# Performance work log

Measured on AMD Instinct MI355X. Metric: run time of the kernel, lower is better.

## Reference

```python
import jax, jax.numpy as jnp
import numpy as np

SEQ_LEN = 4096
D_MODEL = 768
N_Q = 8
Q_DIM = D_MODEL // N_Q  # 96
WINDOW = 128


def apply_rope(x, theta):
    # x: [L, d]; standard rotary embedding on even/odd pairs.
    L = x.shape[0]
    pos = jnp.arange(L, dtype=x.dtype)
    ang = pos[:, None] * theta[None, :]              # [L, d/2]
    cos, sin = jnp.cos(ang), jnp.sin(ang)
    x_even, x_odd = x[:, 0::2], x[:, 1::2]
    out_even = x_even * cos - x_odd * sin
    out_odd = x_even * sin + x_odd * cos
    return jnp.stack([out_even, out_odd], axis=-1).reshape(x.shape)


def setup_inputs() -> dict:
    key = jax.random.key(0)
    kx, kw1, kb1, kw2, kb2 = jax.random.split(key, 5)
    s_in = 1.0 / np.sqrt(D_MODEL)
    return {
        "x": jax.random.normal(kx, (SEQ_LEN, D_MODEL), dtype=jnp.float32),
        "Wqkv": jax.random.normal(kw1, (Q_DIM * (N_Q + 2), D_MODEL), dtype=jnp.float32) * s_in,
        "bqkv": jax.random.normal(kb1, (Q_DIM * (N_Q + 2),), dtype=jnp.float32) * s_in,
        "Wout": jax.random.normal(kw2, (D_MODEL, D_MODEL), dtype=jnp.float32) * s_in,
        "bout": jax.random.normal(kb2, (D_MODEL,), dtype=jnp.float32) * s_in,
    }


def reference(x, Wqkv, bqkv, Wout, bout):
    L = x.shape[0]
    qkv = x @ Wqkv.T + bqkv                                   # [L, 10*Q_DIM]
    k = qkv[:, :Q_DIM]                                        # [L, Q_DIM]
    v = qkv[:, Q_DIM:2 * Q_DIM]                               # [L, Q_DIM]
    q = qkv[:, 2 * Q_DIM:].reshape(L, N_Q, Q_DIM)             # [L, H, Q_DIM]

    theta = 1.0 / 10000.0 ** (jnp.arange(0, Q_DIM, 2, dtype=jnp.float32) / Q_DIM)
    q = jax.vmap(lambda h: apply_rope(h, theta), in_axes=1, out_axes=1)(q)
    k = apply_rope(k, theta)

    # Banded causal mask: j <= i and j > i - WINDOW
    i = jnp.arange(L)[:, None]
    j = jnp.arange(L)[None, :]
    mask = (j <= i) & (j > i - WINDOW)                        # [L, L] bool

    # NOTE: source multiplies by sqrt(q_dim) (faithful to original code).
    scores = jnp.sqrt(jnp.float32(Q_DIM)) * jnp.einsum('ihd,jd->hij', q, k)  # [H, L, L]
    scores = jnp.where(mask[None, :, :], scores, -jnp.inf)
    attn = jax.nn.softmax(scores, axis=2)                     # each row has >=1 valid (diag)

    out = jnp.einsum('hij,jd->hid', attn, v)                  # [H, L, Q_DIM]
    out = out.transpose(1, 0, 2).reshape(L, -1)               # [L, D_MODEL]
    return out @ Wout.T + bout
```

## Files before the change

### kernel.cpp

```cpp
#include <hip/hip_runtime.h>

typedef _Float16 f16;
typedef _Float16 half8 __attribute__((ext_vector_type(8)));
typedef _Float16 f16x2 __attribute__((ext_vector_type(2)));
typedef _Float16 f16x4 __attribute__((ext_vector_type(4)));
typedef float    f32x4 __attribute__((ext_vector_type(4)));

#define DM    768
#define QD    96
#define MFMA16(a,b,c) __builtin_amdgcn_mfma_f32_16x16x32_f16(a, b, c, 0, 0, 0)

__device__ __forceinline__ void async_copy16(const f16* g, f16* l) {
  __builtin_amdgcn_global_load_lds((const __attribute__((address_space(1))) void*)g,
                                   (__attribute__((address_space(3))) void*)l,
                                   16, 0, 0);
}

__global__ __launch_bounds__(256) void prep_kernel(const float* __restrict__ x,
                                                   const float* __restrict__ Wqkv,
                                                   const float* __restrict__ bqkv,
                                                   const float* __restrict__ Wout,
                                                   f16* __restrict__ xh,
                                                   f16* __restrict__ w1h,
                                                   f16* __restrict__ w2h,
                                                   float* __restrict__ b1p,
                                                   float* __restrict__ ctab,
                                                   float* __restrict__ stab) {
  const int NW1 = 1024 * 768 / 4;
  const int NW2 = 768 * 768 / 4;
  int b = blockIdx.x;
  if (b < 3072) {
    int idx = b * 256 + threadIdx.x;
    f32x4 v = ((const f32x4*)x)[idx];
    f16x4 o;
    o[0] = (f16)v[0]; o[1] = (f16)v[1]; o[2] = (f16)v[2]; o[3] = (f16)v[3];
    ((f16x4*)xh)[idx] = o;
    return;
  }
  if (b < 4420) {
    int idx = (b - 3072) * 256 + threadIdx.x;
    if (idx < NW1) {
      int r = idx / 192;
      f16x4 o;
      if (r < 960) {
        f32x4 v = ((const f32x4*)Wqkv)[idx];
        o[0] = (f16)v[0]; o[1] = (f16)v[1]; o[2] = (f16)v[2]; o[3] = (f16)v[3];
      } else {
        o[0] = (f16)0.f; o[1] = (f16)0.f; o[2] = (f16)0.f; o[3] = (f16)0.f;
      }
      ((f16x4*)w1h)[idx] = o;
    } else if (idx < NW1 + NW2) {
      int j = idx - NW1;
      f32x4 v = ((const f32x4*)Wout)[j];
      f16x4 o;
      o[0] = (f16)v[0]; o[1] = (f16)v[1]; o[2] = (f16)v[2]; o[3] = (f16)v[3];
      ((f16x4*)w2h)[j] = o;
    } else {
      int j = idx - (NW1 + NW2);
      b1p[j] = (j < 960) ? bqkv[j] : 0.f;
    }
    return;
  }
  int idx = (b - 4420) * 256 + threadIdx.x;
  int pos = idx >> 6, f = idx & 63;
  if (f < 48) {
    float theta = exp2f((float)f * -0.27682734f);
    float s, c;
    sincosf((float)pos * theta, &s, &c);
    ctab[pos * 48 + f] = c;
    stab[pos * 48 + f] = s;
  }
}

#define GEMM_VM5  asm volatile("s_waitcnt vmcnt(5)" ::: "memory")
#define GEMM_VM0  asm volatile("s_waitcnt vmcnt(0)" ::: "memory")
#define GEMM_SB   __builtin_amdgcn_s_barrier()
#define GEMM_SCB  __builtin_amdgcn_sched_barrier(0)

#define GEMM_STAGE(BUF, K0)                                         \
  do {                                                              \
    async_copy16(Ap + (K0),           lA0 + (BUF) * 2048);          \
    async_copy16(Bp + (K0),           lB0 + (BUF) * 8192);          \
    async_copy16(Bp + 32 * K + (K0),  lB0 + (BUF) * 8192 + 2048);   \
    async_copy16(Bp + 64 * K + (K0),  lB0 + (BUF) * 8192 + 4096);   \
    async_copy16(Bp + 96 * K + (K0),  lB0 + (BUF) * 8192 + 6144);   \
  } while (0)

#define GEMM_COMPUTE(BUF)                                                      \
  do {                                                                         \
    half8 a[2][2], b[2][2];                                                    \
    _Pragma("unroll")                                                          \
    for (int m = 0; m < 2; ++m) {                                              \
      int row = m * 16 + fr;                                                   \
      _Pragma("unroll")                                                        \
      for (int kk = 0; kk < 2; ++kk) {                                         \
        int c = (kk << 2) | kg;                                                \
        a[m][kk] = *(const half8*)&As[BUF][row * 64 + ((c ^ (row & 7)) << 3)]; \
      }                                                                        \
    }                                                                          \
    _Pragma("unroll")                                                          \
    for (int n = 0; n < 2; ++n) {                                              \
      int row = w * 32 + n * 16 + fr;                                          \
      _Pragma("unroll")                                                        \
      for (int kk = 0; kk < 2; ++kk) {                                         \
        int c = (kk << 2) | kg;                                                \
        b[n][kk] = *(const half8*)&Bs[BUF][row * 64 + ((c ^ (row & 7)) << 3)]; \
      }                                                                        \
    }                                                                          \
    _Pragma("unroll")                                                          \
    for (int m = 0; m < 2; ++m)                                                \
      _Pragma("unroll")                                                        \
      for (int n = 0; n < 2; ++n) {                                            \
        acc[m][n] = MFMA16(a[m][0], b[n][0], acc[m][n]);                       \
        acc[m][n] = MFMA16(a[m][1], b[n][1], acc[m][n]);                       \
      }                                                                        \
  } while (0)

#define GEMM_PROLOGUE_AND_LOOP                                      \
  __shared__ f16 As[2][32 * 64];                                    \
  __shared__ f16 Bs[2][128 * 64];                                   \
  const int t  = threadIdx.x;                                       \
  const int bm = blockIdx.x * 32;                                   \
  const int bn = blockIdx.y * 128;                                  \
  const int w  = t >> 6, l = t & 63;                                \
  const int fr = l & 15, kg = l >> 4;                               \
  f32x4 acc[2][2] = {};                                             \
  const int srow = t >> 3;                                          \
  const int skc  = ((t & 7) ^ (srow & 7)) << 3;   \
  const f16* Ap = A + (size_t)(bm + srow) * K + skc;                \
  const f16* Bp = B + (size_t)(bn + srow) * K + skc;                \
  f16* lA0 = &As[0][t * 8];                                         \
  f16* lB0 = &Bs[0][t * 8];                                         \
  const int nt = K >> 6;                                  \
  GEMM_STAGE(0, 0);                                                 \
  GEMM_STAGE(1, 64);                                                \
  for (int tk = 0; tk < nt; ++tk) {                                 \
    if (tk + 1 < nt) { GEMM_VM5; } else { GEMM_VM0; }               \
    GEMM_SB; GEMM_SCB;                                              \
    GEMM_COMPUTE(tk & 1);                                           \
    GEMM_SCB; GEMM_SB;                                              \
    if (tk + 2 < nt) GEMM_STAGE(tk & 1, (tk + 2) << 6);             \
  }

__global__ __launch_bounds__(256) void gemm_f16_tn(const f16* __restrict__ A,
                                                   const f16* __restrict__ B,
                                                   const float* __restrict__ bias,
                                                   float* __restrict__ C,
                                                   int K, int ldc) {
  GEMM_PROLOGUE_AND_LOOP
  const int r0 = kg * 4;
#pragma unroll
  for (int n = 0; n < 2; ++n) {
    int col = bn + w * 32 + n * 16 + fr;
    float bv = bias[col];
#pragma unroll
    for (int m = 0; m < 2; ++m) {
      int row = bm + m * 16 + r0;
#pragma unroll
      for (int r = 0; r < 4; ++r)
        C[(size_t)(row + r) * ldc + col] = acc[m][n][r] + bv;
    }
  }
}

__global__ __launch_bounds__(256) void gemm_qkv_rope(const f16* __restrict__ A,
                                                     const f16* __restrict__ B,
                                                     const float* __restrict__ bias,
                                                     const float* __restrict__ ctab,
                                                     const float* __restrict__ stab,
                                                     f16* __restrict__ qh,
                                                     f16* __restrict__ ql,
                                                     f16* __restrict__ kh,
                                                     f16* __restrict__ kl,
                                                     f16* __restrict__ vT) {
  const int K = 768;
  GEMM_PROLOGUE_AND_LOOP
  const int r0 = kg * 4;
  f16* ls = &As[0][0];
  const int vlo = (bn < 96) ? 96 : bn;
  const int vhi = (bn + 128 < 192) ? (bn + 128) : 192;
  const bool has_v = vlo < vhi;
  const bool even = !(fr & 1);
#pragma unroll
  for (int n = 0; n < 2; ++n) {
    int col = bn + w * 32 + n * 16 + fr;
    float bv = bias[col];
    int seg = (col * 683) >> 16;
    int f = (col - seg * 96) >> 1;
#pragma unroll
    for (int m = 0; m < 2; ++m) {
      int row = bm + m * 16 + r0;
      if (seg == 1) {
        f16x4 pk;
#pragma unroll
        for (int r = 0; r < 4; ++r) pk[r] = (f16)(acc[m][n][r] + bv);
        *(f16x4*)&ls[(col - vlo) * 40 + m * 16 + r0] = pk;
        continue;
      }
#pragma unroll
      for (int r = 0; r < 4; ++r) {
        float v = acc[m][n][r] + bv;
        float p = __shfl_xor(v, 1);
        if (even && col < 960) {
          float c = ctab[(row + r) * 48 + f];
          float s = stab[(row + r) * 48 + f];
          float re = v * c - p * s;
          float ro = v * s + p * c;
          f16 hie = (f16)re, hio = (f16)ro;
          f16x2 hv; hv[0] = hie; hv[1] = hio;
          f16x2 lv; lv[0] = (f16)(re - (float)hie); lv[1] = (f16)(ro - (float)hio);
          if (seg == 0) {
            *(f16x2*)(kh + (size_t)(row + r) * QD + col) = hv;
            *(f16x2*)(kl + (size_t)(row + r) * QD + col) = lv;
          } else {
            int qc = col - 192;
            *(f16x2*)(qh + (size_t)(row + r) * DM + qc) = hv;
            *(f16x2*)(ql + (size_t)(row + r) * DM + qc) = lv;
          }
        }
      }
    }
  }
  if (has_v) {
    __syncthreads();
    const int nv = vhi - vlo;
    for (int idx = t; idx < nv * 4; idx += 256) {
      int cl = idx >> 2, sg = idx & 3;
      *(half8*)(vT + (size_t)(vlo - 96 + cl) * 4096 + bm + sg * 8) =
          *(half8*)&ls[cl * 40 + sg * 8];
    }
  }
}

__global__ __launch_bounds__(256) void attn2_kernel(const f16* __restrict__ qh,
                                                    const f16* __restrict__ ql,
                                                    const f16* __restrict__ kh,
                                                    const f16* __restrict__ kl,
                                                    const f16* __restrict__ vT,
                                                    f16* __restrict__ aout) {
  __shared__ f16 kbuf[192 * 104];
  __shared__ f16 klbuf[192 * 104];
  __shared__ f16 vbuf[96 * 200];
  __shared__ f16 pbuf[4][32 * 40];
  const int t  = threadIdx.x, w = t >> 6, l = t & 63;
  const int fr = l & 15, kg = l >> 4;
  const int i0 = blockIdx.x * 64;
  const int h  = blockIdx.y * 2 + (w >> 1);
  const int q0 = (w & 1) * 32;
  const int jbase = i0 - 128;
  const int nlo = (w & 1) ? 2 : 0;

  for (int it = 0; it < 9; ++it) {
    int c = t + 256 * it;
    int row = c / 12, seg = c - row * 12;
    int jabs = jbase + row; if (jabs < 0) jabs = 0;
    *(half8*)(kbuf + row * 104 + seg * 8) =
        *(const half8*)(kh + (size_t)jabs * QD + seg * 8);
    *(half8*)(klbuf + row * 104 + seg * 8) =
        *(const half8*)(kl + (size_t)jabs * QD + seg * 8);
  }
  for (int it = 0; it < 9; ++it) {
    int c = t + 256 * it;
    int row = c / 24, seg = c - row * 24;
    int col0 = jbase + seg * 8; if (col0 < 0) col0 = 0;
    *(half8*)(vbuf + row * 200 + seg * 8) =
        *(const half8*)(vT + (size_t)row * 4096 + col0);
  }

  half8 a_h[2][3], a_l[2][3];
#pragma unroll
  for (int m = 0; m < 2; ++m) {
    size_t qoff = (size_t)(i0 + q0 + m * 16 + fr) * DM + h * QD;
#pragma unroll
    for (int kc = 0; kc < 3; ++kc) {
      a_h[m][kc] = *(const half8*)(qh + qoff + kc * 32 + kg * 8);
      a_l[m][kc] = *(const half8*)(ql + qoff + kc * 32 + kg * 8);
    }
  }
  __syncthreads();

  f32x4 s[2][12];
#pragma unroll
  for (int m = 0; m < 2; ++m)
#pragma unroll
    for (int n = 0; n < 12; ++n)
      s[m][n] = (f32x4){0.f, 0.f, 0.f, 0.f};

  __builtin_amdgcn_s_setprio(1);
#pragma unroll
  for (int n = 0; n < 12; ++n) {
    if (n < nlo || n >= nlo + 10) continue;
    int krow = n * 16 + fr;
#pragma unroll
    for (int kc = 0; kc < 3; ++kc) {
      half8 b_h = *(const half8*)(kbuf + krow * 104 + kc * 32 + kg * 8);
      half8 b_l = *(const half8*)(klbuf + krow * 104 + kc * 32 + kg * 8);
      s[0][n] = MFMA16(a_h[0][kc], b_h, s[0][n]);
      s[1][n] = MFMA16(a_h[1][kc], b_h, s[1][n]);
      s[0][n] = MFMA16(a_l[0][kc], b_h, s[0][n]);
      s[1][n] = MFMA16(a_l[1][kc], b_h, s[1][n]);
      s[0][n] = MFMA16(a_h[0][kc], b_l, s[0][n]);
      s[1][n] = MFMA16(a_h[1][kc], b_l, s[1][n]);
    }
  }
  __builtin_amdgcn_s_setprio(0);

  const int jmin = (i0 < 128) ? (128 - i0) : 0;
  const float scale = 9.79795897113271f;
  float mx[2][4], sm[2][4], inv[2][4];
#pragma unroll
  for (int m = 0; m < 2; ++m)
#pragma unroll
    for (int r = 0; r < 4; ++r) mx[m][r] = -1e30f;

#pragma unroll
  for (int m = 0; m < 2; ++m)
#pragma unroll
    for (int n = 0; n < 12; ++n) {
      if (n < nlo || n >= nlo + 10) continue;
      int jloc = n * 16 + fr;
#pragma unroll
      for (int r = 0; r < 4; ++r) {
        int iloc = q0 + m * 16 + kg * 4 + r;
        bool valid = (jloc > iloc) && (jloc <= iloc + 128) && (jloc >= jmin);
        float v = valid ? s[m][n][r] * scale : -1e30f;
        s[m][n][r] = v;
        mx[m][r] = fmaxf(mx[m][r], v);
      }
    }
#pragma unroll
  for (int m = 0; m < 2; ++m)
#pragma unroll
    for (int r = 0; r < 4; ++r) {
      float v = mx[m][r];
      v = fmaxf(v, __shfl_xor(v, 1));
      v = fmaxf(v, __shfl_xor(v, 2));
      v = fmaxf(v, __shfl_xor(v, 4));
      v = fmaxf(v, __shfl_xor(v, 8));
      mx[m][r] = v;
      sm[m][r] = 0.f;
    }
#pragma unroll
  for (int m = 0; m < 2; ++m)
#pragma unroll
    for (int n = 0; n < 12; ++n) {
      if (n < nlo || n >= nlo + 10) continue;
#pragma unroll
      for (int r = 0; r < 4; ++r) {
        float p = __expf(s[m][n][r] - mx[m][r]);
        s[m][n][r] = p;
        sm[m][r] += p;
      }
    }
#pragma unroll
  for (int m = 0; m < 2; ++m)
#pragma unroll
    for (int r = 0; r < 4; ++r) {
      float v = sm[m][r];
      v += __shfl_xor(v, 1);
      v += __shfl_xor(v, 2);
      v += __shfl_xor(v, 4);
      v += __shfl_xor(v, 8);
      inv[m][r] = 1.f / v;
    }

  f16* pw = pbuf[w];
  const int c6lo = nlo >> 1;
  f32x4 o[2][6];
#pragma unroll
  for (int m = 0; m < 2; ++m)
#pragma unroll
    for (int dn = 0; dn < 6; ++dn)
      o[m][dn] = (f32x4){0.f, 0.f, 0.f, 0.f};

#pragma unroll
  for (int c6 = 0; c6 < 6; ++c6) {
    if (c6 < c6lo || c6 >= c6lo + 5) continue;
#pragma unroll
    for (int m = 0; m < 2; ++m)
#pragma unroll
      for (int nn = 0; nn < 2; ++nn)
#pragma unroll
        for (int r = 0; r < 4; ++r)
          pw[(m * 16 + kg * 4 + r) * 40 + nn * 16 + fr] = (f16)s[m][2 * c6 + nn][r];
    half8 ap0 = *(half8*)(pw + fr * 40 + kg * 8);
    half8 ap1 = *(half8*)(pw + (16 + fr) * 40 + kg * 8);
    __builtin_amdgcn_s_setprio(1);
#pragma unroll
    for (int dn = 0; dn < 6; ++dn) {
      half8 bv = *(half8*)(vbuf + (dn * 16 + fr) * 200 + c6 * 32 + kg * 8);
      o[0][dn] = MFMA16(ap0, bv, o[0][dn]);
      o[1][dn] = MFMA16(ap1, bv, o[1][dn]);
    }
    __builtin_amdgcn_s_setprio(0);
  }

#pragma unroll
  for (int m = 0; m < 2; ++m)
#pragma unroll
    for (int dn = 0; dn < 6; ++dn) {
      int col = h * QD + dn * 16 + fr;
#pragma unroll
      for (int r = 0; r < 4; ++r) {
        int row = i0 + q0 + m * 16 + kg * 4 + r;
        aout[(size_t)row * DM + col] = (f16)(o[m][dn][r] * inv[m][r]);
      }
    }
}

extern "C" void kernel_launch(void* const* d_in, const int* in_sizes, int n_in,
                              void* d_out, int out_size, void* d_ws, size_t ws_size,
                              hipStream_t stream) {
  const float* x    = (const float*)d_in[0];
  const float* Wqkv = (const float*)d_in[1];
  const float* bqkv = (const float*)d_in[2];
  const float* Wout = (const float*)d_in[3];
  const float* bout = (const float*)d_in[4];
  float* out = (float*)d_out;

  char* ws = (char*)d_ws;
  f16*   xh   = (f16*)(ws);
  f16*   w1h  = (f16*)(ws + 6291456);
  f16*   w2h  = (f16*)(ws + 7864320);
  float* b1p  = (float*)(ws + 9043968);
  float* ctab = (float*)(ws + 9048064);
  float* stab = (float*)(ws + 9834496);
  f16*   qh   = (f16*)(ws + 10620928);
  f16*   ql   = (f16*)(ws + 16912384);
  f16*   kh   = (f16*)(ws + 23203840);
  f16*   kl   = (f16*)(ws + 23990272);
  f16*   vT   = (f16*)(ws + 24776704);
  f16*   aout = (f16*)(ws + 25563136);

  prep_kernel<<<dim3(5444), dim3(256), 0, stream>>>(x, Wqkv, bqkv, Wout,
                                                    xh, w1h, w2h, b1p, ctab, stab);
  gemm_qkv_rope<<<dim3(128, 8), dim3(256), 0, stream>>>(xh, w1h, b1p, ctab, stab,
                                                        qh, ql, kh, kl, vT);
  attn2_kernel<<<dim3(64, 4), dim3(256), 0, stream>>>(qh, ql, kh, kl, vT, aout);
  gemm_f16_tn<<<dim3(128, 6), dim3(256), 0, stream>>>(aout, w2h, bout, out, 768, 768);
}
```

Measured before the change: 54.92 us.

## Load GEMM A operand directly into double-buffered registers, bypassing LDS

The A tile of the shared GEMM mainloop is no longer staged through LDS with async copies. Each lane now reads its MFMA A fragments straight from global memory into two register buffers that alternate between iterations, and the vmcnt wait is retuned to match the new load counts. This removes the LDS writes and reads for A and frees that LDS space; the QKV epilogue now reuses the B buffer as scratch instead. In exchange, all four waves fetch the same A rows, so global/L2 traffic for A rises, the per-lane row-strided loads coalesce less well, and register pressure goes up.

Result: slower. 83.86 us (+52.7%).

```diff
diff --git a/kernel.cpp b/kernel.cpp
--- a/kernel.cpp
+++ b/kernel.cpp
@@ -72,32 +72,32 @@
   }
 }
 
-#define GEMM_VM5  asm volatile("s_waitcnt vmcnt(5)" ::: "memory")
+#define GEMM_VM4  asm volatile("s_waitcnt vmcnt(4)" ::: "memory")
 #define GEMM_VM0  asm volatile("s_waitcnt vmcnt(0)" ::: "memory")
 #define GEMM_SB   __builtin_amdgcn_s_barrier()
 #define GEMM_SCB  __builtin_amdgcn_sched_barrier(0)
 
-#define GEMM_STAGE(BUF, K0)                                         \
+#define GEMM_STAGE_B(BUF, K0)                                       \
   do {                                                              \
-    async_copy16(Ap + (K0),           lA0 + (BUF) * 2048);          \
     async_copy16(Bp + (K0),           lB0 + (BUF) * 8192);          \
     async_copy16(Bp + 32 * K + (K0),  lB0 + (BUF) * 8192 + 2048);   \
     async_copy16(Bp + 64 * K + (K0),  lB0 + (BUF) * 8192 + 4096);   \
     async_copy16(Bp + 96 * K + (K0),  lB0 + (BUF) * 8192 + 6144);   \
   } while (0)
 
-#define GEMM_COMPUTE(BUF)                                                      \
+#define GEMM_LOAD_A(REG, K0)                                        \
+  do {                                                              \
+    _Pragma("unroll")                                               \
+    for (int m = 0; m < 2; ++m)                                     \
+      _Pragma("unroll")                                             \
+      for (int kk = 0; kk < 2; ++kk)                                \
+        REG[m][kk] = *(const half8*)(Aq + (size_t)(m * 16) * K +    \
+                                     (K0) + (((kk << 2) | kg) << 3)); \
+  } while (0)
+
+#define GEMM_COMPUTE(BUF, AREG)                                                \
   do {                                                                         \
-    half8 a[2][2], b[2][2];                                                    \
-    _Pragma("unroll")                                                          \
-    for (int m = 0; m < 2; ++m) {                                              \
-      int row = m * 16 + fr;                                                   \
-      _Pragma("unroll")                                                        \
-      for (int kk = 0; kk < 2; ++kk) {                                         \
-        int c = (kk << 2) | kg;                                                \
-        a[m][kk] = *(const half8*)&As[BUF][row * 64 + ((c ^ (row & 7)) << 3)]; \
-      }                                                                        \
-    }                                                                          \
+    half8 b[2][2];                                                             \
     _Pragma("unroll")                                                          \
     for (int n = 0; n < 2; ++n) {                                              \
       int row = w * 32 + n * 16 + fr;                                          \
@@ -111,13 +111,12 @@
     for (int m = 0; m < 2; ++m)                                                \
       _Pragma("unroll")                                                        \
       for (int n = 0; n < 2; ++n) {                                            \
-        acc[m][n] = MFMA16(a[m][0], b[n][0], acc[m][n]);                       \
-        acc[m][n] = MFMA16(a[m][1], b[n][1], acc[m][n]);                       \
+        acc[m][n] = MFMA16(AREG[m][0], b[n][0], acc[m][n]);                    \
+        acc[m][n] = MFMA16(AREG[m][1], b[n][1], acc[m][n]);                    \
       }                                                                        \
   } while (0)
 
 #define GEMM_PROLOGUE_AND_LOOP                                      \
-  __shared__ f16 As[2][32 * 64];                                    \
   __shared__ f16 Bs[2][128 * 64];                                   \
   const int t  = threadIdx.x;                                       \
   const int bm = blockIdx.x * 32;                                   \
@@ -127,19 +126,24 @@
   f32x4 acc[2][2] = {};                                             \
   const int srow = t >> 3;                                          \
   const int skc  = ((t & 7) ^ (srow & 7)) << 3;   \
-  const f16* Ap = A + (size_t)(bm + srow) * K + skc;                \
   const f16* Bp = B + (size_t)(bn + srow) * K + skc;                \
-  f16* lA0 = &As[0][t * 8];                                         \
+  const f16* Aq = A + (size_t)(bm + fr) * K;                        \
   f16* lB0 = &Bs[0][t * 8];                                         \
-  const int nt = K >> 6;                                  \
-  GEMM_STAGE(0, 0);                                                 \
-  GEMM_STAGE(1, 64);                                                \
+  const int nt = K >> 6;                            \
+  half8 a0[2][2], a1[2][2];                                         \
+  GEMM_STAGE_B(0, 0);                                               \
+  GEMM_LOAD_A(a0, 0);                                               \
+  GEMM_STAGE_B(1, 64);                                              \
   for (int tk = 0; tk < nt; ++tk) {                                 \
-    if (tk + 1 < nt) { GEMM_VM5; } else { GEMM_VM0; }               \
+    if (tk + 1 < nt) { GEMM_VM4; } else { GEMM_VM0; }               \
     GEMM_SB; GEMM_SCB;                                              \
-    GEMM_COMPUTE(tk & 1);                                           \
+    if (tk & 1) { GEMM_COMPUTE(1, a1); } else { GEMM_COMPUTE(0, a0); } \
     GEMM_SCB; GEMM_SB;                                              \
-    if (tk + 2 < nt) GEMM_STAGE(tk & 1, (tk + 2) << 6);             \
+    if (tk + 1 < nt) {                                              \
+      if (tk & 1) { GEMM_LOAD_A(a0, (tk + 1) << 6); }               \
+      else        { GEMM_LOAD_A(a1, (tk + 1) << 6); }               \
+    }                                                               \
+    if (tk + 2 < nt) GEMM_STAGE_B(tk & 1, (tk + 2) << 6);           \
   }
 
 __global__ __launch_bounds__(256) void gemm_f16_tn(const f16* __restrict__ A,
@@ -176,7 +180,7 @@
   const int K = 768;
   GEMM_PROLOGUE_AND_LOOP
   const int r0 = kg * 4;
-  f16* ls = &As[0][0];
+  f16* ls = &Bs[0][0];
   const int vlo = (bn < 96) ? 96 : bn;
   const int vhi = (bn + 128 < 192) ? (bn + 128) : 192;
   const bool has_v = vlo < vhi;
```

## Halve attention query tile per block and shrink LDS footprint

Applied to the files above, without the earlier changes.

The attention kernel now handles 32 query rows per block instead of 64, which doubles the grid to 128x4 blocks and halves the per-wave accumulator registers. The low K part is no longer staged in LDS and is read straight from global memory. The P staging buffer reuses the K buffer after a barrier, which cuts LDS use and should raise occupancy. In exchange, K and V window data is loaded redundantly across more blocks, and the k-low reads from global add latency to the QK MFMA loop.

After: 57.28 us. +4.3%, slower.

```diff
diff --git a/kernel.cpp b/kernel.cpp
--- a/kernel.cpp
+++ b/kernel.cpp
@@ -232,180 +232,159 @@
   }
 }
 
-__global__ __launch_bounds__(256) void attn2_kernel(const f16* __restrict__ qh,
+__global__ __launch_bounds__(256) void attn3_kernel(const f16* __restrict__ qh,
                                                     const f16* __restrict__ ql,
                                                     const f16* __restrict__ kh,
                                                     const f16* __restrict__ kl,
                                                     const f16* __restrict__ vT,
                                                     f16* __restrict__ aout) {
-  __shared__ f16 kbuf[192 * 104];
-  __shared__ f16 klbuf[192 * 104];
-  __shared__ f16 vbuf[96 * 200];
-  __shared__ f16 pbuf[4][32 * 40];
+  __shared__ f16 kbuf[160 * 104];
+  __shared__ f16 vbuf[96 * 168];
   const int t  = threadIdx.x, w = t >> 6, l = t & 63;
   const int fr = l & 15, kg = l >> 4;
-  const int i0 = blockIdx.x * 64;
+  const int i0 = blockIdx.x * 32;
   const int h  = blockIdx.y * 2 + (w >> 1);
-  const int q0 = (w & 1) * 32;
+  const int q0 = (w & 1) * 16;
   const int jbase = i0 - 128;
-  const int nlo = (w & 1) ? 2 : 0;
-
-  for (int it = 0; it < 9; ++it) {
+  const int nlo = w & 1;
+
+  for (int it = 0; it < 8; ++it) {
     int c = t + 256 * it;
-    int row = c / 12, seg = c - row * 12;
-    int jabs = jbase + row; if (jabs < 0) jabs = 0;
-    *(half8*)(kbuf + row * 104 + seg * 8) =
-        *(const half8*)(kh + (size_t)jabs * QD + seg * 8);
-    *(half8*)(klbuf + row * 104 + seg * 8) =
-        *(const half8*)(kl + (size_t)jabs * QD + seg * 8);
-  }
-  for (int it = 0; it < 9; ++it) {
+    if (c < 1920) {
+      int row = c / 12, seg = c - row * 12;
+      int jabs = jbase + row; if (jabs < 0) jabs = 0;
+      *(half8*)(kbuf + row * 104 + seg * 8) =
+          *(const half8*)(kh + (size_t)jabs * QD + seg * 8);
+    }
+  }
+  for (int it = 0; it < 8; ++it) {
     int c = t + 256 * it;
-    int row = c / 24, seg = c - row * 24;
-    int col0 = jbase + seg * 8; if (col0 < 0) col0 = 0;
-    *(half8*)(vbuf + row * 200 + seg * 8) =
-        *(const half8*)(vT + (size_t)row * 4096 + col0);
-  }
-
-  half8 a_h[2][3], a_l[2][3];
-#pragma unroll
-  for (int m = 0; m < 2; ++m) {
-    size_t qoff = (size_t)(i0 + q0 + m * 16 + fr) * DM + h * QD;
+    if (c < 1920) {
+      int row = c / 20, seg = c - row * 20;
+      int col0 = jbase + seg * 8; if (col0 < 0) col0 = 0;
+      *(half8*)(vbuf + row * 168 + seg * 8) =
+          *(const half8*)(vT + (size_t)row * 4096 + col0);
+    }
+  }
+
+  half8 a_h[3], a_l[3];
+  {
+    size_t qoff = (size_t)(i0 + q0 + fr) * DM + h * QD;
 #pragma unroll
     for (int kc = 0; kc < 3; ++kc) {
-      a_h[m][kc] = *(const half8*)(qh + qoff + kc * 32 + kg * 8);
-      a_l[m][kc] = *(const half8*)(ql + qoff + kc * 32 + kg * 8);
+      a_h[kc] = *(const half8*)(qh + qoff + kc * 32 + kg * 8);
+      a_l[kc] = *(const half8*)(ql + qoff + kc * 32 + kg * 8);
     }
   }
   __syncthreads();
 
-  f32x4 s[2][12];
-#pragma unroll
-  for (int m = 0; m < 2; ++m)
-#pragma unroll
-    for (int n = 0; n < 12; ++n)
-      s[m][n] = (f32x4){0.f, 0.f, 0.f, 0.f};
+  f32x4 s[10];
+#pragma unroll
+  for (int n = 0; n < 10; ++n) s[n] = (f32x4){0.f, 0.f, 0.f, 0.f};
 
   __builtin_amdgcn_s_setprio(1);
 #pragma unroll
-  for (int n = 0; n < 12; ++n) {
-    if (n < nlo || n >= nlo + 10) continue;
+  for (int n = 0; n < 10; ++n) {
+    if (n < nlo || n >= nlo + 9) continue;
     int krow = n * 16 + fr;
+    int jabs = jbase + krow; if (jabs < 0) jabs = 0;
 #pragma unroll
     for (int kc = 0; kc < 3; ++kc) {
       half8 b_h = *(const half8*)(kbuf + krow * 104 + kc * 32 + kg * 8);
-      half8 b_l = *(const half8*)(klbuf + krow * 104 + kc * 32 + kg * 8);
-      s[0][n] = MFMA16(a_h[0][kc], b_h, s[0][n]);
-      s[1][n] = MFMA16(a_h[1][kc], b_h, s[1][n]);
-      s[0][n] = MFMA16(a_l[0][kc], b_h, s[0][n]);
-      s[1][n] = MFMA16(a_l[1][kc], b_h, s[1][n]);
-      s[0][n] = MFMA16(a_h[0][kc], b_l, s[0][n]);
-      s[1][n] = MFMA16(a_h[1][kc], b_l, s[1][n]);
+      half8 b_l = *(const half8*)(kl + (size_t)jabs * QD + kc * 32 + kg * 8);
+      s[n] = MFMA16(a_h[kc], b_h, s[n]);
+      s[n] = MFMA16(a_l[kc], b_h, s[n]);
+      s[n] = MFMA16(a_h[kc], b_l, s[n]);
     }
   }
   __builtin_amdgcn_s_setprio(0);
 
   const int jmin = (i0 < 128) ? (128 - i0) : 0;
   const float scale = 9.79795897113271f;
-  float mx[2][4], sm[2][4], inv[2][4];
-#pragma unroll
-  for (int m = 0; m < 2; ++m)
-#pragma unroll
-    for (int r = 0; r < 4; ++r) mx[m][r] = -1e30f;
-
-#pragma unroll
-  for (int m = 0; m < 2; ++m)
-#pragma unroll
-    for (int n = 0; n < 12; ++n) {
-      if (n < nlo || n >= nlo + 10) continue;
-      int jloc = n * 16 + fr;
-#pragma unroll
-      for (int r = 0; r < 4; ++r) {
-        int iloc = q0 + m * 16 + kg * 4 + r;
-        bool valid = (jloc > iloc) && (jloc <= iloc + 128) && (jloc >= jmin);
-        float v = valid ? s[m][n][r] * scale : -1e30f;
-        s[m][n][r] = v;
-        mx[m][r] = fmaxf(mx[m][r], v);
-      }
-    }
-#pragma unroll
-  for (int m = 0; m < 2; ++m)
+  float mx[4], sm[4], inv[4];
+#pragma unroll
+  for (int r = 0; r < 4; ++r) mx[r] = -1e30f;
+
+#pragma unroll
+  for (int n = 0; n < 10; ++n) {
+    if (n < nlo || n >= nlo + 9) continue;
+    int jloc = n * 16 + fr;
 #pragma unroll
     for (int r = 0; r < 4; ++r) {
-      float v = mx[m][r];
-      v = fmaxf(v, __shfl_xor(v, 1));
-      v = fmaxf(v, __shfl_xor(v, 2));
-      v = fmaxf(v, __shfl_xor(v, 4));
-      v = fmaxf(v, __shfl_xor(v, 8));
-      mx[m][r] = v;
-      sm[m][r] = 0.f;
-    }
-#pragma unroll
-  for (int m = 0; m < 2; ++m)
-#pragma unroll
-    for (int n = 0; n < 12; ++n) {
-      if (n < nlo || n >= nlo + 10) continue;
-#pragma unroll
-      for (int r = 0; r < 4; ++r) {
-        float p = __expf(s[m][n][r] - mx[m][r]);
-        s[m][n][r] = p;
-        sm[m][r] += p;
-      }
-    }
-#pragma unroll
-  for (int m = 0; m < 2; ++m)
+      int iloc = q0 + kg * 4 + r;
+      bool valid = (jloc > iloc) && (jloc <= iloc + 128) && (jloc >= jmin);
+      float v = valid ? s[n][r] * scale : -1e30f;
+      s[n][r] = v;
+      mx[r] = fmaxf(mx[r], v);
+    }
+  }
+#pragma unroll
+  for (int r = 0; r < 4; ++r) {
+    float v = mx[r];
+    v = fmaxf(v, __shfl_xor(v, 1));
+    v = fmaxf(v, __shfl_xor(v, 2));
+    v = fmaxf(v, __shfl_xor(v, 4));
+    v = fmaxf(v, __shfl_xor(v, 8));
+    mx[r] = v;
+    sm[r] = 0.f;
+  }
+#pragma unroll
+  for (int n = 0; n < 10; ++n) {
+    if (n < nlo || n >= nlo + 9) {
+#pragma unroll
+      for (int r = 0; r < 4; ++r) s[n][r] = 0.f;
+      continue;
+    }
 #pragma unroll
     for (int r = 0; r < 4; ++r) {
-      float v = sm[m][r];
-      v += __shfl_xor(v, 1);
-      v += __shfl_xor(v, 2);
-      v += __shfl_xor(v, 4);
-      v += __shfl_xor(v, 8);
-      inv[m][r] = 1.f / v;
-    }
-
-  f16* pw = pbuf[w];
-  const int c6lo = nlo >> 1;
-  f32x4 o[2][6];
-#pragma unroll
-  for (int m = 0; m < 2; ++m)
-#pragma unroll
-    for (int dn = 0; dn < 6; ++dn)
-      o[m][dn] = (f32x4){0.f, 0.f, 0.f, 0.f};
-
-#pragma unroll
-  for (int c6 = 0; c6 < 6; ++c6) {
-    if (c6 < c6lo || c6 >= c6lo + 5) continue;
-#pragma unroll
-    for (int m = 0; m < 2; ++m)
-#pragma unroll
-      for (int nn = 0; nn < 2; ++nn)
-#pragma unroll
-        for (int r = 0; r < 4; ++r)
-          pw[(m * 16 + kg * 4 + r) * 40 + nn * 16 + fr] = (f16)s[m][2 * c6 + nn][r];
-    half8 ap0 = *(half8*)(pw + fr * 40 + kg * 8);
-    half8 ap1 = *(half8*)(pw + (16 + fr) * 40 + kg * 8);
+      float p = __expf(s[n][r] - mx[r]);
+      s[n][r] = p;
+      sm[r] += p;
+    }
+  }
+#pragma unroll
+  for (int r = 0; r < 4; ++r) {
+    float v = sm[r];
+    v += __shfl_xor(v, 1);
+    v += __shfl_xor(v, 2);
+    v += __shfl_xor(v, 4);
+    v += __shfl_xor(v, 8);
+    inv[r] = 1.f / v;
+  }
+
+  __syncthreads();
+
+  f16* pw = kbuf + w * 640;
+  f32x4 o[6];
+#pragma unroll
+  for (int dn = 0; dn < 6; ++dn) o[dn] = (f32x4){0.f, 0.f, 0.f, 0.f};
+
+#pragma unroll
+  for (int c6 = 0; c6 < 5; ++c6) {
+#pragma unroll
+    for (int nn = 0; nn < 2; ++nn)
+#pragma unroll
+      for (int r = 0; r < 4; ++r)
+        pw[(kg * 4 + r) * 40 + nn * 16 + fr] = (f16)s[2 * c6 + nn][r];
+    half8 ap = *(half8*)(pw + fr * 40 + kg * 8);
     __builtin_amdgcn_s_setprio(1);
 #pragma unroll
     for (int dn = 0; dn < 6; ++dn) {
-      half8 bv = *(half8*)(vbuf + (dn * 16 + fr) * 200 + c6 * 32 + kg * 8);
-      o[0][dn] = MFMA16(ap0, bv, o[0][dn]);
-      o[1][dn] = MFMA16(ap1, bv, o[1][dn]);
+      half8 bv = *(half8*)(vbuf + (dn * 16 + fr) * 168 + c6 * 32 + kg * 8);
+      o[dn] = MFMA16(ap, bv, o[dn]);
     }
     __builtin_amdgcn_s_setprio(0);
   }
 
 #pragma unroll
-  for (int m = 0; m < 2; ++m)
-#pragma unroll
-    for (int dn = 0; dn < 6; ++dn) {
-      int col = h * QD + dn * 16 + fr;
-#pragma unroll
-      for (int r = 0; r < 4; ++r) {
-        int row = i0 + q0 + m * 16 + kg * 4 + r;
-        aout[(size_t)row * DM + col] = (f16)(o[m][dn][r] * inv[m][r]);
-      }
-    }
+  for (int dn = 0; dn < 6; ++dn) {
+    int col = h * QD + dn * 16 + fr;
+#pragma unroll
+    for (int r = 0; r < 4; ++r) {
+      int row = i0 + q0 + kg * 4 + r;
+      aout[(size_t)row * DM + col] = (f16)(o[dn][r] * inv[r]);
+    }
+  }
 }
 
 extern "C" void kernel_launch(void* const* d_in, const int* in_sizes, int n_in,
@@ -436,6 +415,6 @@
                                                     xh, w1h, w2h, b1p, ctab, stab);
   gemm_qkv_rope<<<dim3(128, 8), dim3(256), 0, stream>>>(xh, w1h, b1p, ctab, stab,
                                                         qh, ql, kh, kl, vT);
-  attn2_kernel<<<dim3(64, 4), dim3(256), 0, stream>>>(qh, ql, kh, kl, vT, aout);
+  attn3_kernel<<<dim3(128, 4), dim3(256), 0, stream>>>(qh, ql, kh, kl, vT, aout);
   gemm_f16_tn<<<dim3(128, 6), dim3(256), 0, stream>>>(aout, w2h, bout, out, 768, 768);
 }
```
